# Performance work log

Measured on AMD Instinct MI355X. Metric: run time of the kernel, lower is better.

## Reference

```python
import jax, jax.numpy as jnp
import numpy as np

N_NODES = 100000
IN_CH = 256
HIDDEN = 256
N_EDGES = 500000


def setup_inputs() -> dict:
    key = jax.random.key(0)
    k_emb, k_ei, k_w1, k_w2 = jax.random.split(key, 4)
    embeddings = jax.random.normal(k_emb, (N_NODES, IN_CH), dtype=jnp.float32)
    edge_index = jax.random.randint(k_ei, (2, N_EDGES), 0, N_NODES, dtype=jnp.int64)
    # Linear(in*2, hidden) and Linear(hidden, 1) weights (stored input-major for x @ W)
    s1 = 1.0 / np.sqrt(2 * IN_CH)
    s2 = 1.0 / np.sqrt(HIDDEN)
    W1 = jax.random.uniform(k_w1, (2 * IN_CH, HIDDEN), dtype=jnp.float32, minval=-s1, maxval=s1)
    b1 = jnp.zeros((HIDDEN,), dtype=jnp.float32)
    W2 = jax.random.uniform(k_w2, (HIDDEN, 1), dtype=jnp.float32, minval=-s2, maxval=s2)
    b2 = jnp.zeros((1,), dtype=jnp.float32)
    return {"embeddings": embeddings, "edge_index": edge_index,
            "W1": W1, "b1": b1, "W2": W2, "b2": b2}


def reference(embeddings, edge_index, W1, b1, W2, b2):
    src, dst = edge_index[0], edge_index[1]
    # gather [E, in] twice, concat -> [E, 2*in]
    feats = jnp.concatenate([embeddings[src], embeddings[dst]], axis=-1)
    h = jax.nn.relu(feats @ W1 + b1)          # [E, hidden]
    scores = h @ W2 + b2                      # [E, 1]
    return scores.reshape(-1)
```

## Files before the change

kernel.cpp:

```cpp
#include <hip/hip_runtime.h>
#include <hip/hip_bf16.h>

#define NN   100000
#define EE   500000
#define MPAD 100096

using bf16x8 = __attribute__((ext_vector_type(8))) short;
using f32x4  = __attribute__((ext_vector_type(4))) float;
using u16x8  = __attribute__((ext_vector_type(8))) unsigned short;

__device__ __forceinline__ unsigned short f2bf(float f) {
  unsigned int x = __builtin_bit_cast(unsigned int, f);
  x += 0x7fffu + ((x >> 16) & 1u);
  return (unsigned short)(x >> 16);
}
__device__ __forceinline__ float bf2f(unsigned short u) {
  unsigned int x = ((unsigned int)u) << 16;
  return __builtin_bit_cast(float, x);
}
__device__ __forceinline__ unsigned short f2bh(float f) {
  return __builtin_bit_cast(unsigned short, __float2bfloat16(f));
}
__device__ __forceinline__ void glds16(const void* g, const void* l) {
  __builtin_amdgcn_global_load_lds((const __attribute__((address_space(1))) void*)g,
                                   (__attribute__((address_space(3))) void*)l, 16, 0, 0);
}

__global__ void wprep_kernel(const float* __restrict__ W1, unsigned short* __restrict__ WT) {
  int id = blockIdx.x * blockDim.x + threadIdx.x;
  if (id >= 512 * 32) return;
  int j  = id >> 5;
  int cg = id & 31;
  int jc = j & 255;
  int kb = (cg << 3) + ((j >= 256) ? 256 : 0);
  u16x8 v;
#pragma unroll
  for (int t = 0; t < 8; ++t)
    v[t] = f2bf(W1[(size_t)(kb + t) * 256 + jc]);
  *reinterpret_cast<u16x8*>(WT + (size_t)j * 256 + (cg << 3)) = v;
}

__global__ __launch_bounds__(256, 3) void gemm_pq(const float* __restrict__ emb,
                                                  const unsigned short* __restrict__ WT,
                                                  const float* __restrict__ b1,
                                                  unsigned short* __restrict__ R) {
  __shared__ float          ldsA[2][128 * 32];
  __shared__ unsigned short ldsB[2][128 * 32];

  const int t    = threadIdx.x;
  const int lane = t & 63;
  const int wave = t >> 6;
  const int wrow = wave >> 1, wcol = wave & 1;
  const int bid = (int)blockIdx.x;
  const int lid = (bid & 7) * 391 + (bid >> 3);
  const int m0 = (lid >> 2) * 128;
  const int n0 = (lid & 3) * 128;

  size_t aOffG[4]; int aLds[4];
#pragma unroll
  for (int i = 0; i < 4; ++i) {
    const int r  = wave * 32 + i * 8 + (lane >> 3);
    const int cp = lane & 7;
    const int g  = cp ^ (r & 7);
    int rg = m0 + r; if (rg >= NN) rg = NN - 1;
    aOffG[i] = (size_t)rg * 256 + (g << 2);
    aLds[i]  = (wave * 32 + i * 8) * 32;
  }
  size_t bOffG[2]; int bLds[2];
#pragma unroll
  for (int i = 0; i < 2; ++i) {
    const int r  = wave * 32 + i * 16 + (lane >> 2);
    const int qp = lane & 3;
    const int g  = qp ^ ((r >> 1) & 3);
    bOffG[i] = (size_t)(n0 + r) * 256 + (g << 3);
    bLds[i]  = (wave * 32 + i * 16) * 32;
  }

  const int fr = lane & 15, fq = lane >> 4;
  int aoff0[4], aoff1[4], boff[4];
#pragma unroll
  for (int m = 0; m < 4; ++m) {
    const int r  = wrow * 64 + 16 * m + fr;
    const int s0 = ((fq << 1) | 0) ^ (r & 7);
    const int s1 = ((fq << 1) | 1) ^ (r & 7);
    aoff0[m] = r * 32 + (s0 << 2);
    aoff1[m] = r * 32 + (s1 << 2);
  }
#pragma unroll
  for (int n = 0; n < 4; ++n) {
    const int r = wcol * 64 + 16 * n + fr;
    boff[n] = r * 32 + ((fq ^ ((r >> 1) & 3)) << 3);
  }

#define STAGE(buf, ks)                                                         \
  do {                                                                         \
    glds16(emb + aOffG[0] + ((ks) << 5), &ldsA[(buf)][aLds[0]]);               \
    glds16(emb + aOffG[1] + ((ks) << 5), &ldsA[(buf)][aLds[1]]);               \
    glds16(emb + aOffG[2] + ((ks) << 5), &ldsA[(buf)][aLds[2]]);               \
    glds16(emb + aOffG[3] + ((ks) << 5), &ldsA[(buf)][aLds[3]]);               \
    glds16(WT + bOffG[0] + ((ks) << 5), &ldsB[(buf)][bLds[0]]);                \
    glds16(WT + bOffG[1] + ((ks) << 5), &ldsB[(buf)][bLds[1]]);                \
  } while (0)

  f32x4 acc[4][4] = {};

  STAGE(0, 0);
  __syncthreads();

#pragma unroll
  for (int ks = 0; ks < 8; ++ks) {
    const int p = ks & 1;
    if (ks < 7) STAGE(p ^ 1, ks + 1);
    bf16x8 av[4], bv[4];
#pragma unroll
    for (int m = 0; m < 4; ++m) {
      const float4 x0 = *(const float4*)&ldsA[p][aoff0[m]];
      const float4 x1 = *(const float4*)&ldsA[p][aoff1[m]];
      bf16x8 a;
      a[0] = (short)f2bh(x0.x); a[1] = (short)f2bh(x0.y);
      a[2] = (short)f2bh(x0.z); a[3] = (short)f2bh(x0.w);
      a[4] = (short)f2bh(x1.x); a[5] = (short)f2bh(x1.y);
      a[6] = (short)f2bh(x1.z); a[7] = (short)f2bh(x1.w);
      av[m] = a;
    }
#pragma unroll
    for (int n = 0; n < 4; ++n) bv[n] = *(const bf16x8*)&ldsB[p][boff[n]];
#pragma unroll
    for (int m = 0; m < 4; ++m)
#pragma unroll
      for (int n = 0; n < 4; ++n)
        acc[m][n] = __builtin_amdgcn_mfma_f32_16x16x32_bf16(av[m], bv[n], acc[m][n], 0, 0, 0);
    if (ks < 7) __syncthreads();
  }

  float bn[4];
#pragma unroll
  for (int n = 0; n < 4; ++n) {
    const int c = n0 + wcol * 64 + 16 * n + fr;
    bn[n] = (c < 256) ? b1[c] : 0.f;
  }
#pragma unroll
  for (int m = 0; m < 4; ++m) {
    const int r0 = m0 + wrow * 64 + 16 * m + (fq << 2);
#pragma unroll
    for (int n = 0; n < 4; ++n) {
      const int c = n0 + wcol * 64 + 16 * n + fr;
#pragma unroll
      for (int i = 0; i < 4; ++i)
        R[(size_t)(r0 + i) * 512 + c] = f2bh(acc[m][n][i] + bn[n]);
    }
  }
#undef STAGE
}

__global__ __launch_bounds__(256) void edge_kernel(const int* __restrict__ idx,
                                                   const unsigned short* __restrict__ R,
                                                   const float* __restrict__ W2,
                                                   const float* __restrict__ b2,
                                                   float* __restrict__ out) {
  const int lane  = threadIdx.x & 63;
  const int half  = lane >> 5;
  const int l     = lane & 31;
  const int gwave = (int)((blockIdx.x * blockDim.x + threadIdx.x) >> 6);
  const int nwave = (int)((gridDim.x * blockDim.x) >> 6);
  const float4 w0 = *(const float4*)(W2 + (l << 3));
  const float4 w1 = *(const float4*)(W2 + (l << 3) + 4);
  const float bias = b2[0];

  for (int c = gwave; c < (EE / 16); c += nwave) {
    const int e0 = c << 4;
    int s[8], d[8];
#pragma unroll
    for (int u = 0; u < 8; ++u) {
      s[u] = idx[e0 + (u << 1) + half];
      d[u] = idx[EE + e0 + (u << 1) + half];
    }
    u16x8 ga[8], gb[8];
#pragma unroll
    for (int u = 0; u < 8; ++u) {
      ga[u] = *(const u16x8*)(R + (size_t)s[u] * 512 + (l << 3));
      gb[u] = *(const u16x8*)(R + (size_t)d[u] * 512 + 256 + (l << 3));
    }
#pragma unroll
    for (int u = 0; u < 8; ++u) {
      float acc;
      acc  = fmaxf(bf2f((unsigned short)ga[u][0]) + bf2f((unsigned short)gb[u][0]), 0.f) * w0.x;
      acc += fmaxf(bf2f((unsigned short)ga[u][1]) + bf2f((unsigned short)gb[u][1]), 0.f) * w0.y;
      acc += fmaxf(bf2f((unsigned short)ga[u][2]) + bf2f((unsigned short)gb[u][2]), 0.f) * w0.z;
      acc += fmaxf(bf2f((unsigned short)ga[u][3]) + bf2f((unsigned short)gb[u][3]), 0.f) * w0.w;
      acc += fmaxf(bf2f((unsigned short)ga[u][4]) + bf2f((unsigned short)gb[u][4]), 0.f) * w1.x;
      acc += fmaxf(bf2f((unsigned short)ga[u][5]) + bf2f((unsigned short)gb[u][5]), 0.f) * w1.y;
      acc += fmaxf(bf2f((unsigned short)ga[u][6]) + bf2f((unsigned short)gb[u][6]), 0.f) * w1.z;
      acc += fmaxf(bf2f((unsigned short)ga[u][7]) + bf2f((unsigned short)gb[u][7]), 0.f) * w1.w;
#pragma unroll
      for (int off = 16; off > 0; off >>= 1) acc += __shfl_xor(acc, off, 64);
      if (l == 0) out[e0 + (u << 1) + half] = acc + bias;
    }
  }
}

__global__ __launch_bounds__(256) void fallback_kernel(const float* __restrict__ emb,
                                                       const int* __restrict__ idx,
                                                       const float* __restrict__ W1,
                                                       const float* __restrict__ b1,
                                                       const float* __restrict__ W2,
                                                       const float* __restrict__ b2,
                                                       float* __restrict__ out) {
  __shared__ float feats[512];
  __shared__ float red[256];
  const int t = threadIdx.x;
  for (int e = blockIdx.x; e < EE; e += gridDim.x) {
    __syncthreads();
    const int s = idx[e], d = idx[EE + e];
    feats[t]       = emb[(size_t)s * 256 + t];
    feats[256 + t] = emb[(size_t)d * 256 + t];
    __syncthreads();
    float h = b1[t];
    for (int k = 0; k < 512; ++k) h += feats[k] * W1[k * 256 + t];
    red[t] = fmaxf(h, 0.f) * W2[t];
    __syncthreads();
    for (int off = 128; off > 0; off >>= 1) {
      if (t < off) red[t] += red[t + off];
      __syncthreads();
    }
    if (t == 0) out[e] = red[0] + b2[0];
  }
}

extern "C" void kernel_launch(void* const* d_in, const int* in_sizes, int n_in,
                              void* d_out, int out_size, void* d_ws, size_t ws_size,
                              hipStream_t stream) {
  const float* emb = (const float*)d_in[0];
  const int*   idx = (const int*)d_in[1];
  const float* W1  = (const float*)d_in[2];
  const float* b1  = (const float*)d_in[3];
  const float* W2  = (const float*)d_in[4];
  const float* b2  = (const float*)d_in[5];
  float* out = (float*)d_out;

  const size_t wt_elems = (size_t)512 * 256;
  const size_t r_elems  = (size_t)MPAD * 512;
  const size_t need = (wt_elems + r_elems) * sizeof(unsigned short);

  if (ws_size < need) {
    fallback_kernel<<<4096, 256, 0, stream>>>(emb, idx, W1, b1, W2, b2, out);
    return;
  }

  unsigned short* WT = (unsigned short*)d_ws;
  unsigned short* R  = WT + wt_elems;

  wprep_kernel<<<64, 256, 0, stream>>>(W1, WT);
  gemm_pq<<<(MPAD / 128) * 4, 256, 0, stream>>>(emb, WT, b1, R);
  edge_kernel<<<2048, 256, 0, stream>>>(idx, R, W2, b2, out);
}
```

Baseline: 133.1 us.

## Bucket-sort edges by source node block to improve gather locality per XCD

Adds a counting-sort pass (histogram, scan, atomic scatter) that groups edges into 128-node source buckets, then runs a new edge kernel that reads the sorted src/dst/permutation arrays. Each XCD gets a contiguous range of sorted chunks, so source-row gathers from the intermediate R table should hit in that XCD's L2. The edge kernels also drop from 8 to 4 edges per lane group. The cost is five extra small launches, an extra pass over the indices with atomics, a scattered write to the output through the permutation, and nondeterministic order within buckets.

```diff
diff --git a/kernel.cpp b/kernel.cpp
--- a/kernel.cpp
+++ b/kernel.cpp
@@ -4,6 +4,8 @@
 #define NN   100000
 #define EE   500000
 #define MPAD 100096
+#define NBKT 782
+#define NCHUNK 62500
 
 using bf16x8 = __attribute__((ext_vector_type(8))) short;
 using f32x4  = __attribute__((ext_vector_type(4))) float;
@@ -38,6 +40,46 @@
   for (int t = 0; t < 8; ++t)
     v[t] = f2bf(W1[(size_t)(kb + t) * 256 + jc]);
   *reinterpret_cast<u16x8*>(WT + (size_t)j * 256 + (cg << 3)) = v;
+}
+
+__global__ __launch_bounds__(256) void zero_bins(int* __restrict__ bins) {
+  for (int i = threadIdx.x; i < NBKT; i += 256) bins[i] = 0;
+}
+__global__ __launch_bounds__(256) void hist_kernel(const int* __restrict__ idx,
+                                                   int* __restrict__ bins) {
+  for (int e = blockIdx.x * blockDim.x + threadIdx.x; e < EE;
+       e += gridDim.x * blockDim.x)
+    atomicAdd(&bins[idx[e] >> 7], 1);
+}
+__global__ __launch_bounds__(1024) void scan_kernel(const int* __restrict__ bins,
+                                                    int* __restrict__ cursor) {
+  __shared__ int sm[1024];
+  const int t = threadIdx.x;
+  const int v0 = (t < NBKT) ? bins[t] : 0;
+  sm[t] = v0;
+  __syncthreads();
+#pragma unroll
+  for (int off = 1; off < 1024; off <<= 1) {
+    int v = (t >= off) ? sm[t - off] : 0;
+    __syncthreads();
+    sm[t] += v;
+    __syncthreads();
+  }
+  if (t < NBKT) cursor[t] = sm[t] - v0;
+}
+__global__ __launch_bounds__(256) void scatter_kernel(const int* __restrict__ idx,
+                                                      int* __restrict__ cursor,
+                                                      int* __restrict__ ss,
+                                                      int* __restrict__ dd,
+                                                      int* __restrict__ pe) {
+  for (int e = blockIdx.x * blockDim.x + threadIdx.x; e < EE;
+       e += gridDim.x * blockDim.x) {
+    const int s = idx[e];
+    const int p = atomicAdd(&cursor[s >> 7], 1);
+    ss[p] = s;
+    dd[p] = idx[EE + e];
+    pe[p] = e;
+  }
 }
 
 __global__ __launch_bounds__(256, 3) void gemm_pq(const float* __restrict__ emb,
@@ -103,7 +145,6 @@
   } while (0)
 
   f32x4 acc[4][4] = {};
-
   STAGE(0, 0);
   __syncthreads();
 
@@ -151,6 +192,59 @@
     }
   }
 #undef STAGE
+}
+
+__global__ __launch_bounds__(256) void edge_sorted(const int* __restrict__ ss,
+                                                   const int* __restrict__ dd,
+                                                   const int* __restrict__ pe,
+                                                   const unsigned short* __restrict__ R,
+                                                   const float* __restrict__ W2,
+                                                   const float* __restrict__ b2,
+                                                   float* __restrict__ out) {
+  const int lane = threadIdx.x & 63;
+  const int half = lane >> 5;
+  const int l    = lane & 31;
+  const int b    = (int)blockIdx.x;
+  const int xcd  = b & 7;
+  const int wl   = (b >> 3) * 4 + (threadIdx.x >> 6);
+  const int base = xcd * 7813;
+  const int cnt  = min(7813, NCHUNK - base);
+  const float4 w0 = *(const float4*)(W2 + (l << 3));
+  const float4 w1 = *(const float4*)(W2 + (l << 3) + 4);
+  const float bias = b2[0];
+
+  for (int c = wl; c < cnt; c += 1024) {
+    const int e0 = (base + c) << 3;
+    int s[4], d[4], o[4];
+#pragma unroll
+    for (int u = 0; u < 4; ++u) {
+      const int ei = e0 + (u << 1) + half;
+      s[u] = ss[ei];
+      d[u] = dd[ei];
+      o[u] = pe[ei];
+    }
+    u16x8 ga[4], gb[4];
+#pragma unroll
+    for (int u = 0; u < 4; ++u) {
+      ga[u] = *(const u16x8*)(R + (size_t)s[u] * 512 + (l << 3));
+      gb[u] = *(const u16x8*)(R + (size_t)d[u] * 512 + 256 + (l << 3));
+    }
+#pragma unroll
+    for (int u = 0; u < 4; ++u) {
+      float acc;
+      acc  = fmaxf(bf2f((unsigned short)ga[u][0]) + bf2f((unsigned short)gb[u][0]), 0.f) * w0.x;
+      acc += fmaxf(bf2f((unsigned short)ga[u][1]) + bf2f((unsigned short)gb[u][1]), 0.f) * w0.y;
+      acc += fmaxf(bf2f((unsigned short)ga[u][2]) + bf2f((unsigned short)gb[u][2]), 0.f) * w0.z;
+      acc += fmaxf(bf2f((unsigned short)ga[u][3]) + bf2f((unsigned short)gb[u][3]), 0.f) * w0.w;
+      acc += fmaxf(bf2f((unsigned short)ga[u][4]) + bf2f((unsigned short)gb[u][4]), 0.f) * w1.x;
+      acc += fmaxf(bf2f((unsigned short)ga[u][5]) + bf2f((unsigned short)gb[u][5]), 0.f) * w1.y;
+      acc += fmaxf(bf2f((unsigned short)ga[u][6]) + bf2f((unsigned short)gb[u][6]), 0.f) * w1.z;
+      acc += fmaxf(bf2f((unsigned short)ga[u][7]) + bf2f((unsigned short)gb[u][7]), 0.f) * w1.w;
+#pragma unroll
+      for (int off = 16; off > 0; off >>= 1) acc += __shfl_xor(acc, off, 64);
+      if (l == 0) out[o[u]] = acc + bias;
+    }
+  }
 }
 
 __global__ __launch_bounds__(256) void edge_kernel(const int* __restrict__ idx,
@@ -166,23 +260,22 @@
   const float4 w0 = *(const float4*)(W2 + (l << 3));
   const float4 w1 = *(const float4*)(W2 + (l << 3) + 4);
   const float bias = b2[0];
-
-  for (int c = gwave; c < (EE / 16); c += nwave) {
-    const int e0 = c << 4;
-    int s[8], d[8];
-#pragma unroll
-    for (int u = 0; u < 8; ++u) {
+  for (int c = gwave; c < (EE / 8); c += nwave) {
+    const int e0 = c << 3;
+    int s[4], d[4];
+#pragma unroll
+    for (int u = 0; u < 4; ++u) {
       s[u] = idx[e0 + (u << 1) + half];
       d[u] = idx[EE + e0 + (u << 1) + half];
     }
-    u16x8 ga[8], gb[8];
-#pragma unroll
-    for (int u = 0; u < 8; ++u) {
+    u16x8 ga[4], gb[4];
+#pragma unroll
+    for (int u = 0; u < 4; ++u) {
       ga[u] = *(const u16x8*)(R + (size_t)s[u] * 512 + (l << 3));
       gb[u] = *(const u16x8*)(R + (size_t)d[u] * 512 + 256 + (l << 3));
     }
 #pragma unroll
-    for (int u = 0; u < 8; ++u) {
+    for (int u = 0; u < 4; ++u) {
       float acc;
       acc  = fmaxf(bf2f((unsigned short)ga[u][0]) + bf2f((unsigned short)gb[u][0]), 0.f) * w0.x;
       acc += fmaxf(bf2f((unsigned short)ga[u][1]) + bf2f((unsigned short)gb[u][1]), 0.f) * w0.y;
@@ -240,17 +333,32 @@
 
   const size_t wt_elems = (size_t)512 * 256;
   const size_t r_elems  = (size_t)MPAD * 512;
-  const size_t need = (wt_elems + r_elems) * sizeof(unsigned short);
-
-  if (ws_size < need) {
-    fallback_kernel<<<4096, 256, 0, stream>>>(emb, idx, W1, b1, W2, b2, out);
-    return;
-  }
+  const size_t base_bytes = (wt_elems + r_elems) * sizeof(unsigned short);
+  const size_t sort_ints  = (size_t)NBKT * 2 + (size_t)EE * 3 + 8;
+  const size_t need_sort  = base_bytes + 16 + sort_ints * sizeof(int);
 
   unsigned short* WT = (unsigned short*)d_ws;
   unsigned short* R  = WT + wt_elems;
-
-  wprep_kernel<<<64, 256, 0, stream>>>(W1, WT);
-  gemm_pq<<<(MPAD / 128) * 4, 256, 0, stream>>>(emb, WT, b1, R);
-  edge_kernel<<<2048, 256, 0, stream>>>(idx, R, W2, b2, out);
-}
+  char* tail = (char*)(R + r_elems);
+  int* bins   = (int*)((((uintptr_t)tail) + 15) & ~(uintptr_t)15);
+  int* cursor = bins + NBKT;
+  int* ss     = cursor + NBKT;
+  int* dd     = ss + EE;
+  int* pe     = dd + EE;
+
+  if (ws_size >= need_sort) {
+    wprep_kernel<<<64, 256, 0, stream>>>(W1, WT);
+    zero_bins<<<1, 256, 0, stream>>>(bins);
+    hist_kernel<<<512, 256, 0, stream>>>(idx, bins);
+    scan_kernel<<<1, 1024, 0, stream>>>(bins, cursor);
+    scatter_kernel<<<512, 256, 0, stream>>>(idx, cursor, ss, dd, pe);
+    gemm_pq<<<(MPAD / 128) * 4, 256, 0, stream>>>(emb, WT, b1, R);
+    edge_sorted<<<2048, 256, 0, stream>>>(ss, dd, pe, R, W2, b2, out);
+  } else if (ws_size >= base_bytes) {
+    wprep_kernel<<<64, 256, 0, stream>>>(W1, WT);
+    gemm_pq<<<(MPAD / 128) * 4, 256, 0, stream>>>(emb, WT, b1, R);
+    edge_kernel<<<2048, 256, 0, stream>>>(idx, R, W2, b2, out);
+  } else {
+    fallback_kernel<<<4096, 256, 0, stream>>>(emb, idx, W1, b1, W2, b2, out);
+  }
+}
```

Result: slower. 356.9 us (+168.2%).
